# Optimization experiments

Measured on AMD Instinct MI355X. Metric: run time of the kernel, lower is better.

The kernel has to match this reference:

```python
import jax, jax.numpy as jnp
import numpy as np
from jax import lax

H, W = 2048, 2048
KS = 3            # spatial NMS / centroid kernel size
EPS_NMS = 1e-5    # NMS3d eps (threshold=0 branch)
EPS_DIV = 1e-8
BORDER = 1        # int(mrSize=1.0)


def _grid_weights():
    # generate_3dgrid(3, 3, 3) centered: coords = linspace(-k/2+1, k/2, k) = [-0.5, 0.5, 1.5]
    c = np.linspace(-KS / 2 + 1, KS / 2, KS).astype(np.float32)
    g2 = np.stack([np.repeat(c, KS), np.tile(c, KS)], 1)                              # [9,2] (y,x), y-major
    g3 = np.concatenate([np.repeat(c, KS * KS)[:, None], np.tile(g2, (KS, 1))], 1)    # [27,3] (z,y,x)
    # grid.t().view(3,3,3,3): out-channel c holds coordinate c over the 3x3x3 cube (OIHW)
    return jnp.asarray(g3.T.reshape(3, 3, KS, KS))


def _border_mask():
    m = np.ones((H, W), np.float32)
    m[:BORDER] = 0; m[H - BORDER:] = 0; m[:, :BORDER] = 0; m[:, W - BORDER:] = 0
    return jnp.asarray(m)


def setup_inputs() -> dict:
    key = jax.random.key(0)
    k1, k2, k3, k4 = jax.random.split(key, 4)
    return {
        "low": jax.random.uniform(k1, (1, 1, H, W), jnp.float32),
        "cur": jax.random.uniform(k2, (1, 1, H, W), jnp.float32),
        "high": jax.random.uniform(k3, (1, 1, H, W), jnp.float32),
        "aff_resp": jax.random.normal(k4, (1, 4, H, W), jnp.float32),
        "octaveMap": jnp.zeros((1, 1, H, W), jnp.float32),
        "num_features": 4096,
    }


def _core(low, cur, high, aff_resp, octaveMap, num_features):
    resp3d = jnp.concatenate([low, cur, high], axis=1)  # [1,3,H,W] scale cube
    # MaxPool3d(kernel=3, stride=1, padding=(0,1,1)) over (scale,H,W) -> [1,1,H,W]
    mp = lax.reduce_window(resp3d, -jnp.inf, lax.max,
                           (1, 3, 3, 3), (1, 1, 1, 1),
                           [(0, 0), (0, 0), (1, 1), (1, 1)])
    nms = (resp3d - mp + EPS_NMS > 0).astype(resp3d.dtype) * resp3d  # broadcast over 3 scales
    # keep only the center scale, zero 1px border, mask already-taken octave positions
    nmsed = nms[:, 1:2] * _border_mask() * (1.0 - octaveMap)          # [1,1,H,W]
    vals, idxs = lax.top_k(nmsed.reshape(-1), num_features)          # fixed-k selection branch
    # centroid fit: coordinate-weighted 3x3x3 sums / mass via conv2d over the 3 scale channels
    gw = _grid_weights()
    num = lax.conv_general_dilated(resp3d, gw, (1, 1), [(1, 1), (1, 1)])
    den = lax.conv_general_dilated(resp3d, jnp.ones((3, 3, KS, KS), resp3d.dtype),
                                   (1, 1), [(1, 1), (1, 1)])
    sc = num / (den + EPS_DIV)  # [1,3,H,W] = (scale, dy, dx)
    yy, xx = jnp.meshgrid(jnp.arange(H, dtype=sc.dtype), jnp.arange(W, dtype=sc.dtype), indexing="ij")
    sc = jnp.stack([sc[0, 0], sc[0, 1] + yy, sc[0, 2] + xx], 0).reshape(3, -1).T  # [H*W,3]
    sc = sc[idxs] / jnp.array([float(min(H, W)), float(H), float(W)], sc.dtype)   # normalize (s,y,x)
    A = aff_resp.reshape(4, -1).T[idxs].reshape(-1, 2, 2)   # gather per-keypoint affine
    A = sc[:, 0][:, None, None] * A                          # scale * A
    center_xy = jnp.stack([sc[:, 2], sc[:, 1]], axis=1)[:, :, None]  # (x, y) column
    lafs = jnp.concatenate([A, center_xy], axis=2)           # [K,2,3] LAFs
    return vals, lafs, nmsed


def reference(low, cur, high, aff_resp, octaveMap, num_features):
    vals, lafs, nmsed = _core(low, cur, high, aff_resp, octaveMap, num_features)
    octave_new = (octaveMap + nmsed).astype(jnp.uint8)  # updated octave occupancy map
    return vals, lafs, octave_new
```

## Files before the change

kernel.cpp:

```cpp
#include <hip/hip_runtime.h>
#include <cstdint>
#include <cstddef>

#define HH 2048
#define WW 2048
#define NPIX (HH * WW)
#define EPS_NMS 1e-5f
#define EPS_DIV 1e-8f
#define NEG_INF (-3.402823466e+38f)
#define ROWS 4
#define LCAP 1024
#define SG_CAP 8192
#define NBIN 2048
#define HIST_BLOCKS 64

typedef unsigned long long u64;


__device__ __forceinline__ float max3(float a, float b, float c) {
    return fmaxf(a, fmaxf(b, c));
}

__global__ __launch_bounds__(256) void nms_map_kernel(
    const float* __restrict__ low, const float* __restrict__ cur,
    const float* __restrict__ high, const float* __restrict__ oct,
    float* __restrict__ oct_out, u64* __restrict__ cand,
    unsigned int* __restrict__ cnt, unsigned int cap)
{
    __shared__ unsigned int lcount, lbase;
    __shared__ u64 lcand[LCAP];

    const int tid = threadIdx.x;
    const int lane = tid & 63;
    const int x4 = blockIdx.x * 1024 + tid * 4;
    const int y0 = blockIdx.y * ROWS;
    if (tid == 0) lcount = 0u;
    __syncthreads();

    float4 L[ROWS + 2], C[ROWS + 2], Hi[ROWS + 2];
    float eL[ROWS + 2][3], eR[ROWS + 2][3];
    #pragma unroll
    for (int r = 0; r < ROWS + 2; ++r) {
        int t = y0 - 1 + r;
        bool valid = (t >= 0) && (t < HH);
        int jj = valid ? (t * WW + x4) : 0;
        if (valid) {
            L[r]  = *(const float4*)(low + jj);
            C[r]  = *(const float4*)(cur + jj);
            Hi[r] = *(const float4*)(high + jj);
        } else {
            L[r] = C[r] = Hi[r] = make_float4(NEG_INF, NEG_INF, NEG_INF, NEG_INF);
        }
        bool doL = valid && (lane == 0) && (x4 > 0);
        bool doR = valid && (lane == 63) && (x4 + 4 < WW);
        eL[r][0] = doL ? low[jj - 1]  : NEG_INF;
        eL[r][1] = doL ? cur[jj - 1]  : NEG_INF;
        eL[r][2] = doL ? high[jj - 1] : NEG_INF;
        eR[r][0] = doR ? low[jj + 4]  : NEG_INF;
        eR[r][1] = doR ? cur[jj + 4]  : NEG_INF;
        eR[r][2] = doR ? high[jj + 4] : NEG_INF;
    }
    float4 O[ROWS];
    #pragma unroll
    for (int j = 0; j < ROWS; ++j)
        O[j] = *(const float4*)(oct + (y0 + j) * WW + x4);

    float4 hz[ROWS + 2], cv[ROWS + 2];
    #pragma unroll
    for (int r = 0; r < ROWS + 2; ++r) {
        int t = y0 - 1 + r;
        bool valid = (t >= 0) && (t < HH);
        float4 z;
        z.x = max3(L[r].x, C[r].x, Hi[r].x);
        z.y = max3(L[r].y, C[r].y, Hi[r].y);
        z.z = max3(L[r].z, C[r].z, Hi[r].z);
        z.w = max3(L[r].w, C[r].w, Hi[r].w);
        float zeL = max3(eL[r][0], eL[r][1], eL[r][2]);
        float zeR = max3(eR[r][0], eR[r][1], eR[r][2]);
        float zl = __shfl_up(z.w, 1, 64);
        float zr = __shfl_down(z.x, 1, 64);
        if (lane == 0)  zl = zeL;
        if (lane == 63) zr = zeR;
        if (valid) {
            hz[r].x = max3(zl,  z.x, z.y);
            hz[r].y = max3(z.x, z.y, z.z);
            hz[r].z = max3(z.y, z.z, z.w);
            hz[r].w = max3(z.z, z.w, zr);
            cv[r] = C[r];
        } else {
            hz[r] = make_float4(NEG_INF, NEG_INF, NEG_INF, NEG_INF);
            cv[r] = make_float4(0.f, 0.f, 0.f, 0.f);
        }
    }

    #pragma unroll
    for (int j = 0; j < ROWS; ++j) {
        int y = y0 + j;
        int idx = y * WW + x4;
        float4 o = O[j];
        float4 c1 = cv[j + 1];
        bool yin = (y > 0) && (y < HH - 1);
        float4 ov;
        #define DO_COMP(comp, i)  {                                               \
            float m = max3(hz[j].comp, hz[j + 1].comp, hz[j + 2].comp);           \
            int xg = x4 + (i);                                                    \
            bool interior = yin && (xg > 0) && (xg < WW - 1);                     \
            float nm = (((c1.comp - m + EPS_NMS) > 0.0f) && interior)             \
                       ? c1.comp * (1.0f - o.comp) : 0.0f;                        \
            ov.comp = (float)((unsigned char)(o.comp + nm));                      \
            if (nm > 0.0f) {                                                      \
                unsigned int p = atomicAdd(&lcount, 1u);                          \
                if (p < LCAP)                                                     \
                    lcand[p] = (((u64)__float_as_uint(nm)) << 32)                 \
                               | (unsigned int)(~(idx + (i)));                    \
            }                                                                     \
        }
        DO_COMP(x, 0) DO_COMP(y, 1) DO_COMP(z, 2) DO_COMP(w, 3)
        #undef DO_COMP
        *(float4*)(oct_out + idx) = ov;
    }

    __syncthreads();
    unsigned int c = lcount < LCAP ? lcount : LCAP;
    if (tid == 0) lbase = atomicAdd(cnt, c);
    __syncthreads();
    unsigned int base = lbase;
    for (unsigned int i = tid; i < c; i += 256) {
        unsigned int p = base + i;
        if (p < cap) cand[p] = lcand[i];
    }
}

__global__ __launch_bounds__(256) void hist_pick_kernel(
    const u64* __restrict__ cand, unsigned int* __restrict__ cnt,
    unsigned int* __restrict__ hist, unsigned int cap, int pass, int K)
{
    __shared__ unsigned int h[NBIN];
    __shared__ unsigned int s[256];
    __shared__ bool amLast;
    int tid = threadIdx.x;
    for (int i = tid; i < NBIN; i += 256) h[i] = 0u;
    __syncthreads();
    unsigned int n = cnt[0]; if (n > cap) n = cap;
    unsigned int prefix = cnt[3];
    unsigned int stride = gridDim.x * blockDim.x;
    for (unsigned int i = blockIdx.x * blockDim.x + tid; i < n; i += stride) {
        unsigned int k32 = (unsigned int)(cand[i] >> 32);
        if (pass == 0) {
            atomicAdd(&h[k32 >> 21], 1u);
        } else if ((k32 >> 21) == prefix) {
            atomicAdd(&h[(k32 >> 10) & (NBIN - 1u)], 1u);
        }
    }
    __syncthreads();
    for (int i = tid; i < NBIN; i += 256) { unsigned int v = h[i]; if (v) atomicAdd(&hist[i], v); }
    __threadfence();
    if (tid == 0) amLast = (atomicAdd(&cnt[8 + pass], 1u) == gridDim.x - 1u);
    __syncthreads();
    if (!amLast) return;
    __threadfence();

    unsigned int bins[8], csum = 0;
    #pragma unroll
    for (int i = 0; i < 8; ++i) { bins[i] = hist[tid * 8 + i]; csum += bins[i]; }
    s[tid] = csum;
    __syncthreads();
    for (int off = 1; off < 256; off <<= 1) {
        unsigned int v = (tid + off < 256) ? s[tid + off] : 0u;
        __syncthreads();
        s[tid] += v;
        __syncthreads();
    }
    unsigned int remk = (pass == 0) ? (unsigned int)K : cnt[4];
    unsigned int incl = s[tid];
    unsigned int excl = incl - csum;
    unsigned int total = s[0];
    if (incl >= remk && excl < remk) {
        unsigned int cum = excl;
        int b = 7;
        for (; b > 0; --b) { cum += bins[b]; if (cum >= remk) break; }
        if (cum < remk) cum += bins[0];
        cnt[3] = (prefix << 11) | (unsigned int)(tid * 8 + b);
        cnt[4] = remk - (cum - bins[b]);
    }
    if (tid == 0 && total < remk)
        cnt[3] = (prefix << 11);
    for (int i = tid; i < NBIN; i += 256) hist[i] = 0u;
}

__global__ __launch_bounds__(256) void compact_kernel(
    const u64* __restrict__ cand, u64* __restrict__ SG,
    unsigned int* __restrict__ cnt, unsigned int cap)
{
    __shared__ unsigned int lc, lb;
    __shared__ u64 buf[2048];
    int tid = threadIdx.x;
    unsigned int n = cnt[0]; if (n > cap) n = cap;
    unsigned int T = cnt[3];
    if (tid == 0) lc = 0u;
    __syncthreads();
    unsigned int stride = gridDim.x * blockDim.x;
    for (unsigned int i = blockIdx.x * blockDim.x + tid; i < n; i += stride) {
        u64 key = cand[i];
        if (((unsigned int)(key >> 32) >> 10) >= T) {
            unsigned int p = atomicAdd(&lc, 1u);
            if (p < 2048u) buf[p] = key;
        }
    }
    __syncthreads();
    unsigned int c = lc < 2048u ? lc : 2048u;
    if (tid == 0) lb = atomicAdd(&cnt[1], c);
    __syncthreads();
    unsigned int base = lb;
    for (unsigned int i = tid; i < c; i += 256) {
        unsigned int p = base + i;
        if (p < SG_CAP) SG[p] = buf[i];
    }
}

__global__ __launch_bounds__(256) void rank_finalize_kernel(
    const u64* __restrict__ SG, const unsigned int* __restrict__ cnt,
    const float* __restrict__ low, const float* __restrict__ cur,
    const float* __restrict__ high, const float* __restrict__ aff,
    float* __restrict__ out, int K)
{
    unsigned int m = cnt[1]; if (m > SG_CAP) m = SG_CAP;
    unsigned int wave = threadIdx.x >> 6;
    unsigned int lane = threadIdx.x & 63u;
    unsigned int e = blockIdx.x * 4 + wave;
    if (e >= m) return;
    u64 my = SG[e];

    unsigned int rank = 0;
    for (unsigned int j = lane; j < m; j += 64)
        rank += (unsigned)(SG[j] > my);
    #pragma unroll
    for (int off = 32; off > 0; off >>= 1)
        rank += __shfl_down(rank, off, 64);
    if (lane != 0) return;
    if (rank >= (unsigned int)K) return;

    float val = __uint_as_float((unsigned int)(my >> 32));
    unsigned int idx = ~((unsigned int)my);
    out[rank] = val;
    float* laf = out + K + (size_t)rank * 6;
    int y = (int)(idx >> 11), x = (int)(idx & (WW - 1));
    const float ccw[3] = {-0.5f, 0.5f, 1.5f};
    float den = 0.0f, nz = 0.0f, ny = 0.0f, nx = 0.0f;
    #pragma unroll
    for (int dy = -1; dy <= 1; ++dy) {
        int yy = y + dy;
        if (yy < 0 || yy >= HH) continue;
        #pragma unroll
        for (int dx = -1; dx <= 1; ++dx) {
            int xx = x + dx;
            if (xx < 0 || xx >= WW) continue;
            int jj = yy * WW + xx;
            float v0 = low[jj], v1 = cur[jj], v2 = high[jj];
            float ssum = v0 + v1 + v2;
            den += ssum;
            nz += -0.5f * v0 + 0.5f * v1 + 1.5f * v2;
            ny += ccw[dy + 1] * ssum;
            nx += ccw[dx + 1] * ssum;
        }
    }
    float inv = 1.0f / (den + EPS_DIV);
    float s_n = (nz * inv) * (1.0f / 2048.0f);
    float y_n = (ny * inv + (float)y) * (1.0f / 2048.0f);
    float x_n = (nx * inv + (float)x) * (1.0f / 2048.0f);
    float a0 = aff[idx], a1 = aff[NPIX + idx], a2 = aff[2 * NPIX + idx], a3 = aff[3 * NPIX + idx];
    laf[0] = s_n * a0; laf[1] = s_n * a1; laf[2] = x_n;
    laf[3] = s_n * a2; laf[4] = s_n * a3; laf[5] = y_n;
}

extern "C" void kernel_launch(void* const* d_in, const int* in_sizes, int n_in,
                              void* d_out, int out_size, void* d_ws, size_t ws_size,
                              hipStream_t stream) {
    const float* low  = (const float*)d_in[0];
    const float* cur  = (const float*)d_in[1];
    const float* high = (const float*)d_in[2];
    const float* aff  = (const float*)d_in[3];
    const float* oct  = (const float*)d_in[4];
    int K = (out_size - NPIX) / 7;
    float* out = (float*)d_out;

    char* ws = (char*)d_ws;
    unsigned int* cnt  = (unsigned int*)ws;
    unsigned int* hist = (unsigned int*)(ws + 64);
    u64* SG            = (u64*)(ws + 16384);
    const size_t cand_off = 81920;
    u64* cand          = (u64*)(ws + cand_off);
    size_t cap_sz = ws_size > cand_off ? (ws_size - cand_off) / 8 : 0;
    if (cap_sz > (size_t)NPIX) cap_sz = (size_t)NPIX;
    unsigned int cap = (unsigned int)cap_sz;

    hipMemsetAsync(ws, 0, 64 + NBIN * 4, stream);
    hipMemsetAsync(out, 0, (size_t)7 * K * sizeof(float), stream);

    dim3 gb(WW / 1024, HH / ROWS, 1);
    nms_map_kernel<<<gb, 256, 0, stream>>>(low, cur, high, oct, out + (size_t)7 * K, cand, cnt, cap);

    hist_pick_kernel<<<HIST_BLOCKS, 256, 0, stream>>>(cand, cnt, hist, cap, 0, K);
    hist_pick_kernel<<<HIST_BLOCKS, 256, 0, stream>>>(cand, cnt, hist, cap, 1, K);
    compact_kernel<<<64, 256, 0, stream>>>(cand, SG, cnt, cap);
    rank_finalize_kernel<<<SG_CAP / 4, 256, 0, stream>>>(SG, cnt, low, cur, high, aff, out, K);
}
```

Baseline: 211.6 us.

## Fuse histogram passes and compaction into one persistent kernel with grid barriers

Merges the two radix-histogram selection launches and the compaction launch into a single 64-block kernel that synchronises through spin-wait grid barriers on global counters. The zeroing of the output values region moves into the NMS kernel, and the global histogram is cleared inside the kernel, so two memsets and two launches go away. This cuts launch and memset overhead between the small selection stages. It depends on all 64 blocks being resident at the same time, otherwise the spin barriers can deadlock.

Measured after the change: 212.0 us. Within noise of the previous version (+0.2%).

```diff
diff --git a/kernel.cpp b/kernel.cpp
--- a/kernel.cpp
+++ b/kernel.cpp
@@ -12,20 +12,35 @@
 #define LCAP 1024
 #define SG_CAP 8192
 #define NBIN 2048
-#define HIST_BLOCKS 64
+#define SEL_BLOCKS 64
 
 typedef unsigned long long u64;
 
 
 __device__ __forceinline__ float max3(float a, float b, float c) {
     return fmaxf(a, fmaxf(b, c));
+}
+
+__device__ __forceinline__ unsigned int aload(const unsigned int* p) {
+    return __hip_atomic_load(p, __ATOMIC_RELAXED, __HIP_MEMORY_SCOPE_AGENT);
+}
+
+__device__ __forceinline__ void gbar(unsigned int* ctr) {
+    __syncthreads();
+    if (threadIdx.x == 0) {
+        __threadfence();
+        atomicAdd(ctr, 1u);
+        while (aload(ctr) < (unsigned int)SEL_BLOCKS) {}
+        __threadfence();
+    }
+    __syncthreads();
 }
 
 __global__ __launch_bounds__(256) void nms_map_kernel(
     const float* __restrict__ low, const float* __restrict__ cur,
     const float* __restrict__ high, const float* __restrict__ oct,
-    float* __restrict__ oct_out, u64* __restrict__ cand,
-    unsigned int* __restrict__ cnt, unsigned int cap)
+    float* __restrict__ oct_out, float* __restrict__ vals_out, int n7k,
+    u64* __restrict__ cand, unsigned int* __restrict__ cnt, unsigned int cap)
 {
     __shared__ unsigned int lcount, lbase;
     __shared__ u64 lcand[LCAP];
@@ -35,6 +50,13 @@
     const int x4 = blockIdx.x * 1024 + tid * 4;
     const int y0 = blockIdx.y * ROWS;
     if (tid == 0) lcount = 0u;
+
+    if (blockIdx.y == 0) {
+        int n4 = n7k >> 2;
+        float4* vz = (float4*)vals_out;
+        for (int i = blockIdx.x * 256 + tid; i < n4; i += gridDim.x * 256)
+            vz[i] = make_float4(0.f, 0.f, 0.f, 0.f);
+    }
     __syncthreads();
 
     float4 L[ROWS + 2], C[ROWS + 2], Hi[ROWS + 2];
@@ -131,78 +153,103 @@
     }
 }
 
-__global__ __launch_bounds__(256) void hist_pick_kernel(
-    const u64* __restrict__ cand, unsigned int* __restrict__ cnt,
-    unsigned int* __restrict__ hist, unsigned int cap, int pass, int K)
+__global__ __launch_bounds__(256) void select_kernel(
+    const u64* __restrict__ cand, u64* __restrict__ SG,
+    unsigned int* __restrict__ cnt, unsigned int* __restrict__ hist,
+    unsigned int cap, int K)
 {
     __shared__ unsigned int h[NBIN];
     __shared__ unsigned int s[256];
-    __shared__ bool amLast;
-    int tid = threadIdx.x;
-    for (int i = tid; i < NBIN; i += 256) h[i] = 0u;
-    __syncthreads();
-    unsigned int n = cnt[0]; if (n > cap) n = cap;
-    unsigned int prefix = cnt[3];
-    unsigned int stride = gridDim.x * blockDim.x;
-    for (unsigned int i = blockIdx.x * blockDim.x + tid; i < n; i += stride) {
-        unsigned int k32 = (unsigned int)(cand[i] >> 32);
-        if (pass == 0) {
-            atomicAdd(&h[k32 >> 21], 1u);
-        } else if ((k32 >> 21) == prefix) {
-            atomicAdd(&h[(k32 >> 10) & (NBIN - 1u)], 1u);
-        }
-    }
-    __syncthreads();
-    for (int i = tid; i < NBIN; i += 256) { unsigned int v = h[i]; if (v) atomicAdd(&hist[i], v); }
-    __threadfence();
-    if (tid == 0) amLast = (atomicAdd(&cnt[8 + pass], 1u) == gridDim.x - 1u);
-    __syncthreads();
-    if (!amLast) return;
-    __threadfence();
-
-    unsigned int bins[8], csum = 0;
-    #pragma unroll
-    for (int i = 0; i < 8; ++i) { bins[i] = hist[tid * 8 + i]; csum += bins[i]; }
-    s[tid] = csum;
-    __syncthreads();
-    for (int off = 1; off < 256; off <<= 1) {
-        unsigned int v = (tid + off < 256) ? s[tid + off] : 0u;
-        __syncthreads();
-        s[tid] += v;
-        __syncthreads();
-    }
-    unsigned int remk = (pass == 0) ? (unsigned int)K : cnt[4];
-    unsigned int incl = s[tid];
-    unsigned int excl = incl - csum;
-    unsigned int total = s[0];
-    if (incl >= remk && excl < remk) {
-        unsigned int cum = excl;
-        int b = 7;
-        for (; b > 0; --b) { cum += bins[b]; if (cum >= remk) break; }
-        if (cum < remk) cum += bins[0];
-        cnt[3] = (prefix << 11) | (unsigned int)(tid * 8 + b);
-        cnt[4] = remk - (cum - bins[b]);
-    }
-    if (tid == 0 && total < remk)
-        cnt[3] = (prefix << 11);
-    for (int i = tid; i < NBIN; i += 256) hist[i] = 0u;
-}
-
-__global__ __launch_bounds__(256) void compact_kernel(
-    const u64* __restrict__ cand, u64* __restrict__ SG,
-    unsigned int* __restrict__ cnt, unsigned int cap)
-{
+    __shared__ unsigned int sh_prefix, sh_remk;
     __shared__ unsigned int lc, lb;
     __shared__ u64 buf[2048];
-    int tid = threadIdx.x;
+    const int tid = threadIdx.x;
+    const int bid = blockIdx.x;
+    unsigned int* bar = cnt + 16;
     unsigned int n = cnt[0]; if (n > cap) n = cap;
-    unsigned int T = cnt[3];
+    const unsigned int stride = SEL_BLOCKS * 256;
+
+    int gtid = bid * 256 + tid;
+    if (gtid < NBIN) hist[gtid] = 0u;
+    for (int i = tid; i < NBIN; i += 256) h[i] = 0u;
+    __syncthreads();
+
+    for (unsigned int i = bid * 256 + tid; i < n; i += stride)
+        atomicAdd(&h[(unsigned int)(cand[i] >> 53)], 1u);
+    gbar(&bar[0]);
+    for (int i = tid; i < NBIN; i += 256) { unsigned int v = h[i]; if (v) atomicAdd(&hist[i], v); }
+    gbar(&bar[1]);
+
+    if (bid == 0) {
+        unsigned int bins[8], csum = 0;
+        #pragma unroll
+        for (int i = 0; i < 8; ++i) { bins[i] = aload(&hist[tid * 8 + i]); csum += bins[i]; }
+        s[tid] = csum;
+        __syncthreads();
+        for (int off = 1; off < 256; off <<= 1) {
+            unsigned int v = (tid + off < 256) ? s[tid + off] : 0u;
+            __syncthreads(); s[tid] += v; __syncthreads();
+        }
+        unsigned int remk = (unsigned int)K;
+        unsigned int incl = s[tid], excl = incl - csum, total = s[0];
+        if (incl >= remk && excl < remk) {
+            unsigned int cum = excl; int b = 7;
+            for (; b > 0; --b) { cum += bins[b]; if (cum >= remk) break; }
+            if (cum < remk) cum += bins[0];
+            sh_prefix = (unsigned int)(tid * 8 + b);
+            sh_remk   = remk - (cum - bins[b]);
+        }
+        if (tid == 0 && total < remk) { sh_prefix = 0u; sh_remk = remk; }
+        __syncthreads();
+        for (int i = tid; i < NBIN; i += 256) hist[i] = 0u;
+        __syncthreads();
+        if (tid == 0) atomicExch(&cnt[3], sh_prefix);
+    }
+    gbar(&bar[2]);
+
+    unsigned int prefix = aload(&cnt[3]);
+    for (int i = tid; i < NBIN; i += 256) h[i] = 0u;
+    __syncthreads();
+    for (unsigned int i = bid * 256 + tid; i < n; i += stride) {
+        unsigned int k32 = (unsigned int)(cand[i] >> 32);
+        if ((k32 >> 21) == prefix) atomicAdd(&h[(k32 >> 10) & (NBIN - 1u)], 1u);
+    }
+    __syncthreads();
+    for (int i = tid; i < NBIN; i += 256) { unsigned int v = h[i]; if (v) atomicAdd(&hist[i], v); }
+    gbar(&bar[3]);
+
+    if (bid == 0) {
+        unsigned int bins[8], csum = 0;
+        #pragma unroll
+        for (int i = 0; i < 8; ++i) { bins[i] = aload(&hist[tid * 8 + i]); csum += bins[i]; }
+        s[tid] = csum;
+        __syncthreads();
+        for (int off = 1; off < 256; off <<= 1) {
+            unsigned int v = (tid + off < 256) ? s[tid + off] : 0u;
+            __syncthreads(); s[tid] += v; __syncthreads();
+        }
+        unsigned int remk = sh_remk, pfx = sh_prefix;
+        unsigned int incl = s[tid], excl = incl - csum, total = s[0];
+        __shared__ unsigned int sh_T;
+        if (tid == 0) sh_T = pfx << 11;
+        __syncthreads();
+        if (incl >= remk && excl < remk) {
+            unsigned int cum = excl; int b = 7;
+            for (; b > 0; --b) { cum += bins[b]; if (cum >= remk) break; }
+            if (cum < remk) cum += bins[0];
+            sh_T = (pfx << 11) | (unsigned int)(tid * 8 + b);
+        }
+        __syncthreads();
+        if (tid == 0) atomicExch(&cnt[3], sh_T);
+    }
+    gbar(&bar[4]);
+
+    unsigned int T = aload(&cnt[3]);
     if (tid == 0) lc = 0u;
     __syncthreads();
-    unsigned int stride = gridDim.x * blockDim.x;
-    for (unsigned int i = blockIdx.x * blockDim.x + tid; i < n; i += stride) {
+    for (unsigned int i = bid * 256 + tid; i < n; i += stride) {
         u64 key = cand[i];
-        if (((unsigned int)(key >> 32) >> 10) >= T) {
+        if ((unsigned int)(key >> 42) >= T) {
             unsigned int p = atomicAdd(&lc, 1u);
             if (p < 2048u) buf[p] = key;
         }
@@ -286,7 +333,7 @@
 
     char* ws = (char*)d_ws;
     unsigned int* cnt  = (unsigned int*)ws;
-    unsigned int* hist = (unsigned int*)(ws + 64);
+    unsigned int* hist = (unsigned int*)(ws + 128);
     u64* SG            = (u64*)(ws + 16384);
     const size_t cand_off = 81920;
     u64* cand          = (u64*)(ws + cand_off);
@@ -294,14 +341,11 @@
     if (cap_sz > (size_t)NPIX) cap_sz = (size_t)NPIX;
     unsigned int cap = (unsigned int)cap_sz;
 
-    hipMemsetAsync(ws, 0, 64 + NBIN * 4, stream);
-    hipMemsetAsync(out, 0, (size_t)7 * K * sizeof(float), stream);
+    hipMemsetAsync(ws, 0, 128, stream);
 
     dim3 gb(WW / 1024, HH / ROWS, 1);
-    nms_map_kernel<<<gb, 256, 0, stream>>>(low, cur, high, oct, out + (size_t)7 * K, cand, cnt, cap);
-
-    hist_pick_kernel<<<HIST_BLOCKS, 256, 0, stream>>>(cand, cnt, hist, cap, 0, K);
-    hist_pick_kernel<<<HIST_BLOCKS, 256, 0, stream>>>(cand, cnt, hist, cap, 1, K);
-    compact_kernel<<<64, 256, 0, stream>>>(cand, SG, cnt, cap);
+    nms_map_kernel<<<gb, 256, 0, stream>>>(low, cur, high, oct, out + (size_t)7 * K,
+                                           out, 7 * K, cand, cnt, cap);
+    select_kernel<<<SEL_BLOCKS, 256, 0, stream>>>(cand, SG, cnt, hist, cap, K);
     rank_finalize_kernel<<<SG_CAP / 4, 256, 0, stream>>>(SG, cnt, low, cur, high, aff, out, K);
 }
```
